# Kernel optimization log

Measured on AMD Instinct MI355X. Metric: run time of the kernel, lower is better.

## Reference

```python
import jax, jax.numpy as jnp
import numpy as np

B, C, R, E = 8192, 32, 24, 128
NUM_LOC = 100000
NUM_INNER = 200000   # inner_node_embed has NUM_INNER+1 rows; row 0 is padding_idx
NUM_SLICES = 24


def setup_inputs() -> dict:
    key = jax.random.key(0)
    ks = jax.random.split(key, 7)
    context = jax.random.randint(ks[0], (B, C), 0, NUM_LOC)
    route = jax.random.randint(ks[1], (B, R), 0, NUM_INNER + 1)
    lr = jax.random.randint(ks[2], (B, R), 0, 2)
    slice_idx = jax.random.randint(ks[3], (B,), 0, NUM_SLICES)
    input_embed = jax.random.normal(ks[4], (NUM_LOC, E), dtype=jnp.float32)
    inner_node_embed = jax.random.normal(ks[5], (NUM_INNER + 1, E), dtype=jnp.float32).at[0].set(0.0)
    slice_node_embed = jax.random.uniform(ks[6], (NUM_SLICES, E), dtype=jnp.float32)
    return {
        "context": context, "route": route, "lr": lr, "slice_idx": slice_idx,
        "input_embed": input_embed, "inner_node_embed": inner_node_embed,
        "slice_node_embed": slice_node_embed,
    }


def reference(context, route, lr, slice_idx, input_embed, inner_node_embed, slice_node_embed):
    # context embedding: gather + sum over context window -> (B, E)
    ctx = input_embed[context].sum(axis=1)
    # slice prediction: (B, num_slices) softmax, gather target slice prob -> (B,)
    slice_logits = jnp.einsum('se,be->bs', slice_node_embed, ctx)
    slice_prob = jax.nn.softmax(slice_logits, axis=1)
    slice_pre = jnp.take_along_axis(slice_prob, slice_idx[:, None], axis=1)[:, 0]
    # route scores: (B, R)
    dot = jnp.einsum('bre,be->br', inner_node_embed[route], ctx)
    lr_pre = jax.nn.sigmoid(dot)
    # (2p)^lr - p  -> p if lr==1, (1-p) if lr==0
    route_hidden = jnp.power(2.0 * lr_pre, lr.astype(lr_pre.dtype)) - lr_pre
    # padded route positions (route id == 0) contribute factor 1
    route_hidden = jnp.where(route == 0, jnp.ones((), lr_pre.dtype), route_hidden)
    # per-level product loop collapsed into a single prod over route dim
    pr_route = slice_pre * jnp.prod(route_hidden, axis=1)
    return 1.0 - pr_route.mean()
```

## Files before the change

### kernel.cpp

```cpp
#include <hip/hip_runtime.h>

#define BATCH    8192
#define CTX      32
#define ROUTES   24
#define EDIM     128
#define NSLICE   24
#define WAVES_PER_BLOCK 4

__global__ __launch_bounds__(256) void tale_main(
    const int* __restrict__ context,
    const int* __restrict__ route,
    const int* __restrict__ lr,
    const int* __restrict__ slice_idx,
    const float* __restrict__ input_embed,
    const float* __restrict__ inner_node_embed,
    const float* __restrict__ slice_node_embed,
    float* __restrict__ ws_sum)
{
    const int lane = threadIdx.x & 63;
    const int waveInBlock = threadIdx.x >> 6;
    const int b = blockIdx.x * WAVES_PER_BLOCK + waveInBlock;

    __shared__ float blockSums[WAVES_PER_BLOCK];

    int cidx = 0, ridx = 0, lridx = 0;
    if (lane < CTX) cidx = context[b * CTX + lane];
    if (lane < ROUTES) {
        ridx  = route[b * ROUTES + lane];
        lridx = lr[b * ROUTES + lane];
    }
    const int si = slice_idx[b];

    float2 ctx = make_float2(0.f, 0.f);
    #pragma unroll
    for (int c = 0; c < CTX; ++c) {
        const int idx = __shfl(cidx, c);
        const float2 v = *reinterpret_cast<const float2*>(
            &input_embed[(size_t)idx * EDIM + 2 * lane]);
        ctx.x += v.x;
        ctx.y += v.y;
    }

    float m = -3.0e38f;
    float d = 0.f;
    float sel = 0.f;
    #pragma unroll
    for (int s = 0; s < NSLICE; ++s) {
        const float2 w = *reinterpret_cast<const float2*>(
            &slice_node_embed[s * EDIM + 2 * lane]);
        float p = w.x * ctx.x + w.y * ctx.y;
        #pragma unroll
        for (int off = 32; off > 0; off >>= 1) p += __shfl_xor(p, off);
        const float mNew = fmaxf(m, p);
        d = d * __expf(m - mNew) + __expf(p - mNew);
        m = mNew;
        if (s == si) sel = p;
    }
    const float slice_pre = __expf(sel - m) / d;

    float prod = 1.f;
    #pragma unroll
    for (int r = 0; r < ROUTES; ++r) {
        const int idx = __shfl(ridx, r);
        const int l   = __shfl(lridx, r);
        const float2 v = *reinterpret_cast<const float2*>(
            &inner_node_embed[(size_t)idx * EDIM + 2 * lane]);
        float p = v.x * ctx.x + v.y * ctx.y;
        #pragma unroll
        for (int off = 32; off > 0; off >>= 1) p += __shfl_xor(p, off);
        const float sg = 1.f / (1.f + __expf(-p));
        float h = l ? sg : (1.f - sg);
        if (idx == 0) h = 1.f;
        prod *= h;
    }

    const float pr = slice_pre * prod;

    if (lane == 0) blockSums[waveInBlock] = pr;
    __syncthreads();
    if (threadIdx.x == 0) {
        float s = 0.f;
        #pragma unroll
        for (int w = 0; w < WAVES_PER_BLOCK; ++w) s += blockSums[w];
        atomicAdd(ws_sum, s);
    }
}

__global__ void tale_finalize(const float* __restrict__ ws_sum,
                              float* __restrict__ out)
{
    out[0] = 1.0f - ws_sum[0] * (1.0f / (float)BATCH);
}

extern "C" void kernel_launch(void* const* d_in, const int* in_sizes, int n_in,
                              void* d_out, int out_size, void* d_ws, size_t ws_size,
                              hipStream_t stream)
{
    const int*   context          = (const int*)  d_in[0];
    const int*   route            = (const int*)  d_in[1];
    const int*   lr               = (const int*)  d_in[2];
    const int*   slice_idx        = (const int*)  d_in[3];
    const float* input_embed      = (const float*)d_in[4];
    const float* inner_node_embed = (const float*)d_in[5];
    const float* slice_node_embed = (const float*)d_in[6];
    float* out = (float*)d_out;
    float* ws  = (float*)d_ws;

    hipMemsetAsync(ws, 0, sizeof(float), stream);

    tale_main<<<BATCH / WAVES_PER_BLOCK, 64 * WAVES_PER_BLOCK, 0, stream>>>(
        context, route, lr, slice_idx,
        input_embed, inner_node_embed, slice_node_embed, ws);

    tale_finalize<<<1, 1, 0, stream>>>(ws, out);
}
```

Baseline: 211.3 us.

## Use float4 half-wave gathers and fold finalize into fused atomic output

Each wave is split into two 32-lane halves, each loading 16-byte float4 rows, so every half-wave gathers a whole embedding row and two rows are in flight per instruction. The context sum, route dots and slice softmax are each split across the halves and merged with cross-half shuffles, which shortens the reduction trees to five steps. The separate finalize kernel is dropped by having each block atomically add its share of 1 - mean directly into the output, and launch bounds now request higher occupancy. The per-block constant-offset atomics change floating-point summation order slightly.

```diff
diff --git a/kernel.cpp b/kernel.cpp
--- a/kernel.cpp
+++ b/kernel.cpp
@@ -5,9 +5,10 @@
 #define ROUTES   24
 #define EDIM     128
 #define NSLICE   24
-#define WAVES_PER_BLOCK 4
+#define WPB      4
+#define NBLOCKS  (BATCH / WPB)
 
-__global__ __launch_bounds__(256) void tale_main(
+__global__ __launch_bounds__(256, 8) void tale_fused(
     const int* __restrict__ context,
     const int* __restrict__ route,
     const int* __restrict__ lr,
@@ -15,13 +16,16 @@
     const float* __restrict__ input_embed,
     const float* __restrict__ inner_node_embed,
     const float* __restrict__ slice_node_embed,
-    float* __restrict__ ws_sum)
+    float* __restrict__ out)
 {
-    const int lane = threadIdx.x & 63;
-    const int waveInBlock = threadIdx.x >> 6;
-    const int b = blockIdx.x * WAVES_PER_BLOCK + waveInBlock;
+    const int tid  = threadIdx.x;
+    const int lane = tid & 63;
+    const int half = lane >> 5;
+    const int sub  = lane & 31;
+    const int w    = tid >> 6;
+    const int b    = blockIdx.x * WPB + w;
 
-    __shared__ float blockSums[WAVES_PER_BLOCK];
+    __shared__ float bs[WPB];
 
     int cidx = 0, ridx = 0, lridx = 0;
     if (lane < CTX) cidx = context[b * CTX + lane];
@@ -31,65 +35,72 @@
     }
     const int si = slice_idx[b];
 
-    float2 ctx = make_float2(0.f, 0.f);
+    float4 acc = make_float4(0.f, 0.f, 0.f, 0.f);
     #pragma unroll
-    for (int c = 0; c < CTX; ++c) {
-        const int idx = __shfl(cidx, c);
-        const float2 v = *reinterpret_cast<const float2*>(
-            &input_embed[(size_t)idx * EDIM + 2 * lane]);
-        ctx.x += v.x;
-        ctx.y += v.y;
+    for (int i = 0; i < 16; ++i) {
+        const int idx = __shfl(cidx, i + (half << 4));
+        const float4 v = *reinterpret_cast<const float4*>(
+            input_embed + (size_t)idx * EDIM + (sub << 2));
+        acc.x += v.x; acc.y += v.y; acc.z += v.z; acc.w += v.w;
     }
+    acc.x += __shfl_xor(acc.x, 32);
+    acc.y += __shfl_xor(acc.y, 32);
+    acc.z += __shfl_xor(acc.z, 32);
+    acc.w += __shfl_xor(acc.w, 32);
 
-    float m = -3.0e38f;
-    float d = 0.f;
-    float sel = 0.f;
+    float prodv = 1.f;
     #pragma unroll
-    for (int s = 0; s < NSLICE; ++s) {
-        const float2 w = *reinterpret_cast<const float2*>(
-            &slice_node_embed[s * EDIM + 2 * lane]);
-        float p = w.x * ctx.x + w.y * ctx.y;
-        #pragma unroll
-        for (int off = 32; off > 0; off >>= 1) p += __shfl_xor(p, off);
-        const float mNew = fmaxf(m, p);
-        d = d * __expf(m - mNew) + __expf(p - mNew);
-        m = mNew;
-        if (s == si) sel = p;
-    }
-    const float slice_pre = __expf(sel - m) / d;
-
-    float prod = 1.f;
-    #pragma unroll
-    for (int r = 0; r < ROUTES; ++r) {
-        const int idx = __shfl(ridx, r);
-        const int l   = __shfl(lridx, r);
-        const float2 v = *reinterpret_cast<const float2*>(
-            &inner_node_embed[(size_t)idx * EDIM + 2 * lane]);
-        float p = v.x * ctx.x + v.y * ctx.y;
-        #pragma unroll
-        for (int off = 32; off > 0; off >>= 1) p += __shfl_xor(p, off);
+    for (int i = 0; i < 12; ++i) {
+        const int d   = 2 * i + half;
+        const int idx = __shfl(ridx, d);
+        const int l   = __shfl(lridx, d);
+        const float4 v = *reinterpret_cast<const float4*>(
+            inner_node_embed + (size_t)idx * EDIM + (sub << 2));
+        float p = v.x * acc.x + v.y * acc.y + v.z * acc.z + v.w * acc.w;
+        p += __shfl_xor(p, 16);
+        p += __shfl_xor(p, 8);
+        p += __shfl_xor(p, 4);
+        p += __shfl_xor(p, 2);
+        p += __shfl_xor(p, 1);
         const float sg = 1.f / (1.f + __expf(-p));
         float h = l ? sg : (1.f - sg);
         if (idx == 0) h = 1.f;
-        prod *= h;
+        prodv *= h;
     }
+    prodv *= __shfl_xor(prodv, 32);
 
-    const float pr = slice_pre * prod;
+    float m = -3.0e38f, den = 0.f, selv = 0.f;
+    #pragma unroll
+    for (int i = 0; i < 12; ++i) {
+        const int s = 2 * i + half;
+        const float4 v = *reinterpret_cast<const float4*>(
+            slice_node_embed + s * EDIM + (sub << 2));
+        float p = v.x * acc.x + v.y * acc.y + v.z * acc.z + v.w * acc.w;
+        p += __shfl_xor(p, 16);
+        p += __shfl_xor(p, 8);
+        p += __shfl_xor(p, 4);
+        p += __shfl_xor(p, 2);
+        p += __shfl_xor(p, 1);
+        const float mN = fmaxf(m, p);
+        den = den * __expf(m - mN) + __expf(p - mN);
+        m = mN;
+        if (s == si) selv = p;
+    }
+    const float m_o   = __shfl_xor(m, 32);
+    const float den_o = __shfl_xor(den, 32);
+    const float M     = fmaxf(m, m_o);
+    const float dtot  = den * __expf(m - M) + den_o * __expf(m_o - M);
+    const float sel   = __shfl(selv, (si & 1) << 5);
+    const float slice_pre = __expf(sel - M) / dtot;
 
-    if (lane == 0) blockSums[waveInBlock] = pr;
+    const float pr = slice_pre * prodv;
+
+    if (lane == 0) bs[w] = pr;
     __syncthreads();
-    if (threadIdx.x == 0) {
-        float s = 0.f;
-        #pragma unroll
-        for (int w = 0; w < WAVES_PER_BLOCK; ++w) s += blockSums[w];
-        atomicAdd(ws_sum, s);
+    if (tid == 0) {
+        const float s = bs[0] + bs[1] + bs[2] + bs[3];
+        atomicAdd(out, 1.0f / NBLOCKS - s * (1.0f / BATCH));
     }
-}
-
-__global__ void tale_finalize(const float* __restrict__ ws_sum,
-                              float* __restrict__ out)
-{
-    out[0] = 1.0f - ws_sum[0] * (1.0f / (float)BATCH);
 }
 
 extern "C" void kernel_launch(void* const* d_in, const int* in_sizes, int n_in,
@@ -104,13 +115,10 @@
     const float* inner_node_embed = (const float*)d_in[5];
     const float* slice_node_embed = (const float*)d_in[6];
     float* out = (float*)d_out;
-    float* ws  = (float*)d_ws;
 
-    hipMemsetAsync(ws, 0, sizeof(float), stream);
+    hipMemsetAsync(out, 0, sizeof(float), stream);
 
-    tale_main<<<BATCH / WAVES_PER_BLOCK, 64 * WAVES_PER_BLOCK, 0, stream>>>(
+    tale_fused<<<NBLOCKS, 64 * WPB, 0, stream>>>(
         context, route, lr, slice_idx,
-        input_embed, inner_node_embed, slice_node_embed, ws);
-
-    tale_finalize<<<1, 1, 0, stream>>>(ws, out);
+        input_embed, inner_node_embed, slice_node_embed, out);
 }
```

After: 207.1 us. -2.0%, faster.
